# Performance work log

Hardware: AMD Instinct MI355X
Metric: run time of the kernel (lower is better)

## Reference

```python
import jax, jax.numpy as jnp
import numpy as np

EPS = 1e-12  # matches torch F.normalize eps

def _l2norm(x):
    n = jnp.linalg.norm(x, axis=-1, keepdims=True)
    return x / jnp.maximum(n, EPS)

def setup_inputs() -> dict:
    key = jax.random.key(0)
    k1, k2, k3, k4, k5 = jax.random.split(key, 5)
    B, S, D, V, N = 8, 512, 128, 100000, 2048
    query_embeddings = jax.random.normal(k1, (B, S, D), dtype=jnp.float32)
    key_embeddings = jax.random.normal(k2, (V, D), dtype=jnp.float32)
    batch_idx = jax.random.randint(k3, (N, 1), 0, B)
    seq_idx = jax.random.randint(k4, (N, 1), 0, S)
    label_locations = jnp.concatenate([batch_idx, seq_idx], axis=1).astype(jnp.int64)
    labels = jax.random.randint(k5, (N,), 0, V).astype(jnp.int64)
    return {"query_embeddings": query_embeddings, "key_embeddings": key_embeddings,
            "label_locations": label_locations, "labels": labels}

def reference(query_embeddings, key_embeddings, label_locations, labels):
    # gather supervised positions: [N, D]
    q = query_embeddings[label_locations[:, 0], label_locations[:, 1]]
    q = _l2norm(q)
    k = _l2norm(key_embeddings)
    logits = jnp.einsum('nd,vd->nv', q, k)  # [N, V]
    # mean-reduced softmax cross entropy
    logz = jax.nn.logsumexp(logits, axis=-1)  # [N]
    tgt = jnp.take_along_axis(logits, labels[:, None], axis=-1)[:, 0]
    return jnp.mean(logz - tgt)
```

## Files before the change

kernel.cpp:

```cpp
#include <hip/hip_runtime.h>
#include <hip/hip_bf16.h>

typedef __attribute__((ext_vector_type(8))) short short8;
typedef __attribute__((ext_vector_type(4))) short short4v;
typedef __attribute__((ext_vector_type(4))) float f32x4;

namespace {
constexpr int D    = 128;
constexpr int SEQ  = 512;
constexpr int NV   = 100000;
constexpr int NN   = 2048;
constexpr int KC   = 64;
constexpr int CHUNK_B = KC * D * 2;
constexpr int NCHUNK  = (NV + KC - 1) / KC;
constexpr int CPS     = 17;
constexpr int NSLICE  = (NCHUNK + CPS - 1) / CPS;
constexpr int MBLKS   = 8;
constexpr float LOG2E = 1.4426950408889634f;
constexpr float EPSN  = 1e-12f;
}

__global__ __launch_bounds__(256)
void prep_kernel(const float* __restrict__ qemb,
                 const float* __restrict__ kemb,
                 const int*   __restrict__ loc,
                 __hip_bfloat16* __restrict__ Kn,
                 __hip_bfloat16* __restrict__ Qn)
{
    const int gw   = (blockIdx.x * blockDim.x + threadIdx.x) >> 6;
    const int lane = threadIdx.x & 63;
    const int half = lane >> 5;
    const int l32  = lane & 31;
    const int row  = gw * 2 + half;
    if (row >= NV + NN) return;

    const float* src;
    __hip_bfloat16* dst;
    float extra;
    if (row < NV) {
        src = kemb + (size_t)row * D;
        dst = Kn + (size_t)row * D;
        extra = 1.0f;
    } else {
        int n = row - NV;
        int b = loc[2 * n], s = loc[2 * n + 1];
        src = qemb + ((size_t)b * SEQ + s) * D;
        dst = Qn + (size_t)n * D;
        extra = LOG2E;
    }
    float4 v = *(const float4*)(src + l32 * 4);
    float ss = v.x * v.x + v.y * v.y + v.z * v.z + v.w * v.w;
    #pragma unroll
    for (int m = 1; m < 32; m <<= 1) ss += __shfl_xor(ss, m);
    float inv = extra / fmaxf(sqrtf(ss), EPSN);

    union { __hip_bfloat162 h2[2]; short4v s4; } u;
    u.h2[0].x = __float2bfloat16(v.x * inv);
    u.h2[0].y = __float2bfloat16(v.y * inv);
    u.h2[1].x = __float2bfloat16(v.z * inv);
    u.h2[1].y = __float2bfloat16(v.w * inv);
    *(short4v*)((char*)dst + l32 * 8) = u.s4;
}

__global__ __launch_bounds__(512, 4)
void lse_main(const __hip_bfloat16* __restrict__ Kn,
              const __hip_bfloat16* __restrict__ Qn,
              float* __restrict__ sums)
{
    __shared__ char lds[3 * CHUNK_B];
    const int tid  = threadIdx.x;
    const int lane = tid & 63;
    const int lr   = lane & 15;
    const int lh   = lane >> 4;
    const int w    = tid >> 6;

    const int bid = blockIdx.x;
    const int lin = (bid & 7) * NSLICE + (bid >> 3);
    const int slice = lin >> 3;
    const int mblk  = lin & 7;

    const int chunk0 = slice * CPS;
    const int nch = min(CPS, NCHUNK - chunk0);
    const int m0 = mblk * 256 + w * 32;
    const char* kbase = (const char*)Kn;

    auto stage = [&](int c, int bi) {
        const int keybase = (chunk0 + c) * KC;
        #pragma unroll
        for (int r = 0; r < 2; ++r) {
            const int i   = w * 2 + r;
            const int kic = i * 4 + lh;
            const int key = min(keybase + kic, NV - 1);
            const int sb  = (lr ^ (kic & 7)) << 4;
            const char* g = kbase + (size_t)key * 256 + sb;
            const char* l = lds + bi * CHUNK_B + i * 1024;
            __builtin_amdgcn_global_load_lds(
                (const __attribute__((address_space(1))) void*)g,
                (__attribute__((address_space(3))) void*)l, 16, 0, 0);
        }
    };

    stage(0, 0);
    if (nch > 1) stage(1, 1);

    short8 qf[2][4];
    #pragma unroll
    for (int rg = 0; rg < 2; ++rg)
        #pragma unroll
        for (int ds = 0; ds < 4; ++ds)
            qf[rg][ds] = *(const short8*)((const short*)Qn +
                          (size_t)(m0 + rg * 16 + lr) * D + ds * 32 + lh * 8);

    float rowsum[2][4] = {};
    __syncthreads();

    for (int c = 0; c < nch; ++c) {
        if (c + 2 < nch) stage(c + 2, (c + 2) % 3);

        const char* buf = lds + (c % 3) * CHUNK_B;
        const int vbase = (chunk0 + c) * KC;
        const bool full = (vbase + KC <= NV);
        #pragma unroll
        for (int kg = 0; kg < 4; ++kg) {
            const int kic = kg * 16 + lr;
            const int rx  = (kic & 7) << 4;
            f32x4 acc[2] = {{0,0,0,0},{0,0,0,0}};
            #pragma unroll
            for (int ds2 = 0; ds2 < 4; ++ds2) {
                short8 bf = *(const short8*)(buf +
                              ((kic * 256 + ds2 * 64 + lh * 16) ^ rx));
                #pragma unroll
                for (int rg = 0; rg < 2; ++rg)
                    acc[rg] = __builtin_amdgcn_mfma_f32_16x16x32_bf16(
                                  qf[rg][ds2], bf, acc[rg], 0, 0, 0);
            }
            if (full) {
                #pragma unroll
                for (int rg = 0; rg < 2; ++rg)
                    #pragma unroll
                    for (int j = 0; j < 4; ++j)
                        rowsum[rg][j] += __builtin_amdgcn_exp2f(acc[rg][j]);
            } else {
                const bool ok = (vbase + kic) < NV;
                #pragma unroll
                for (int rg = 0; rg < 2; ++rg)
                    #pragma unroll
                    for (int j = 0; j < 4; ++j)
                        rowsum[rg][j] += ok ? __builtin_amdgcn_exp2f(acc[rg][j]) : 0.f;
            }
        }
        asm volatile("s_waitcnt vmcnt(2)" ::: "memory");
        __builtin_amdgcn_s_barrier();
        asm volatile("" ::: "memory");
    }

    #pragma unroll
    for (int rg = 0; rg < 2; ++rg)
        #pragma unroll
        for (int j = 0; j < 4; ++j) {
            float v = rowsum[rg][j];
            v += __shfl_xor(v, 1);
            v += __shfl_xor(v, 2);
            v += __shfl_xor(v, 4);
            v += __shfl_xor(v, 8);
            if (lr == 0)
                atomicAdd(&sums[m0 + rg * 16 + lh * 4 + j], v);
        }
}

__global__ void tgt_kernel(const float* __restrict__ qemb,
                           const float* __restrict__ kemb,
                           const int*   __restrict__ loc,
                           const int*   __restrict__ labels,
                           float* __restrict__ tgt)
{
    int n = (blockIdx.x * blockDim.x + threadIdx.x) >> 6;
    int lane = threadIdx.x & 63;
    if (n >= NN) return;
    int b = loc[2 * n], s = loc[2 * n + 1];
    const float* q = qemb + ((size_t)b * SEQ + s) * D;
    const float* k = kemb + (size_t)labels[n] * D;
    float2 qv = *(const float2*)(q + lane * 2);
    float2 kv = *(const float2*)(k + lane * 2);
    float qq = qv.x * qv.x + qv.y * qv.y;
    float kk = kv.x * kv.x + kv.y * kv.y;
    float qk = qv.x * kv.x + qv.y * kv.y;
    #pragma unroll
    for (int m = 1; m < 64; m <<= 1) {
        qq += __shfl_xor(qq, m);
        kk += __shfl_xor(kk, m);
        qk += __shfl_xor(qk, m);
    }
    if (lane == 0)
        tgt[n] = qk / (fmaxf(sqrtf(qq), EPSN) * fmaxf(sqrtf(kk), EPSN));
}

__global__ void final_kernel(const float* __restrict__ sums,
                             const float* __restrict__ tgt,
                             float* __restrict__ out)
{
    __shared__ float wsum[4];
    int t = threadIdx.x;
    float acc = 0.f;
    for (int n = t; n < NN; n += 256)
        acc += logf(sums[n]) - tgt[n];
    #pragma unroll
    for (int m = 1; m < 64; m <<= 1) acc += __shfl_xor(acc, m);
    if ((t & 63) == 0) wsum[t >> 6] = acc;
    __syncthreads();
    if (t == 0) out[0] = (wsum[0] + wsum[1] + wsum[2] + wsum[3]) / (float)NN;
}

extern "C" void kernel_launch(void* const* d_in, const int* in_sizes, int n_in,
                              void* d_out, int out_size, void* d_ws, size_t ws_size,
                              hipStream_t stream)
{
    const float* qemb   = (const float*)d_in[0];
    const float* kemb   = (const float*)d_in[1];
    const int*   loc    = (const int*)d_in[2];
    const int*   labels = (const int*)d_in[3];
    float* out = (float*)d_out;

    char* ws = (char*)d_ws;
    __hip_bfloat16* Kn = (__hip_bfloat16*)ws;
    size_t off = (size_t)NV * D * 2;
    __hip_bfloat16* Qn = (__hip_bfloat16*)(ws + off);
    off += (size_t)NN * D * 2;
    float* sums = (float*)(ws + off); off += (size_t)NN * 4;
    float* tgt  = (float*)(ws + off); off += (size_t)NN * 4;

    hipMemsetAsync(sums, 0, NN * sizeof(float), stream);

    {
        int waves  = (NV + NN + 1) / 2;
        int blocks = (waves + 3) / 4;
        prep_kernel<<<blocks, 256, 0, stream>>>(qemb, kemb, loc, Kn, Qn);
    }
    lse_main<<<MBLKS * NSLICE, 512, 0, stream>>>(Kn, Qn, sums);
    tgt_kernel<<<(NN * 64 + 255) / 256, 256, 0, stream>>>(qemb, kemb, loc, labels, tgt);
    final_kernel<<<1, 256, 0, stream>>>(sums, tgt, out);
}
```

Baseline: 161.0 us.

## Fuse target/final kernels into prep and main, enlarge per-wave tile and pipeline depth

The memset, target-logit kernel and final reduction kernel are removed. Zeroing and target dot products move into the prep kernel, and the final mean is computed by the last block of the LSE kernel using an atomic ticket counter. The main kernel now uses 256 threads with each wave covering 64 query rows, which doubles reuse of each staged key fragment. It also uses a four-buffer LDS pipeline with three chunks in flight and fixed slices of 25 chunks. This cuts launch overhead and LDS reads per MFMA, at the cost of more registers, larger LDS per block and a grid-wide completion counter.

```diff
diff --git a/kernel.cpp b/kernel.cpp
--- a/kernel.cpp
+++ b/kernel.cpp
@@ -12,10 +12,10 @@
 constexpr int NN   = 2048;
 constexpr int KC   = 64;
 constexpr int CHUNK_B = KC * D * 2;
-constexpr int NCHUNK  = (NV + KC - 1) / KC;
-constexpr int CPS     = 17;
-constexpr int NSLICE  = (NCHUNK + CPS - 1) / CPS;
+constexpr int CPS     = 25;
+constexpr int NSLICE  = 63;
 constexpr int MBLKS   = 8;
+constexpr int GRID    = MBLKS * NSLICE;
 constexpr float LOG2E = 1.4426950408889634f;
 constexpr float EPSN  = 1e-12f;
 }
@@ -24,50 +24,75 @@
 void prep_kernel(const float* __restrict__ qemb,
                  const float* __restrict__ kemb,
                  const int*   __restrict__ loc,
+                 const int*   __restrict__ labels,
                  __hip_bfloat16* __restrict__ Kn,
-                 __hip_bfloat16* __restrict__ Qn)
+                 __hip_bfloat16* __restrict__ Qn,
+                 float* __restrict__ tgt,
+                 float* __restrict__ sums,
+                 unsigned int* __restrict__ counter)
 {
-    const int gw   = (blockIdx.x * blockDim.x + threadIdx.x) >> 6;
+    const int gid = blockIdx.x * blockDim.x + threadIdx.x;
+    if (gid < NN) sums[gid] = 0.f;
+    if (gid == NN) *counter = 0u;
+
+    const int gw   = gid >> 6;
     const int lane = threadIdx.x & 63;
     const int half = lane >> 5;
     const int l32  = lane & 31;
     const int row  = gw * 2 + half;
     if (row >= NV + NN) return;
 
-    const float* src;
-    __hip_bfloat16* dst;
-    float extra;
     if (row < NV) {
-        src = kemb + (size_t)row * D;
-        dst = Kn + (size_t)row * D;
-        extra = 1.0f;
+        const float* src = kemb + (size_t)row * D;
+        float4 v = *(const float4*)(src + l32 * 4);
+        float ss = v.x * v.x + v.y * v.y + v.z * v.z + v.w * v.w;
+        #pragma unroll
+        for (int m = 1; m < 32; m <<= 1) ss += __shfl_xor(ss, m);
+        float inv = 1.0f / fmaxf(sqrtf(ss), EPSN);
+        union { __hip_bfloat162 h2[2]; short4v s4; } u;
+        u.h2[0].x = __float2bfloat16(v.x * inv);
+        u.h2[0].y = __float2bfloat16(v.y * inv);
+        u.h2[1].x = __float2bfloat16(v.z * inv);
+        u.h2[1].y = __float2bfloat16(v.w * inv);
+        *(short4v*)((char*)(Kn + (size_t)row * D) + l32 * 8) = u.s4;
     } else {
-        int n = row - NV;
-        int b = loc[2 * n], s = loc[2 * n + 1];
-        src = qemb + ((size_t)b * SEQ + s) * D;
-        dst = Qn + (size_t)n * D;
-        extra = LOG2E;
-    }
-    float4 v = *(const float4*)(src + l32 * 4);
-    float ss = v.x * v.x + v.y * v.y + v.z * v.z + v.w * v.w;
-    #pragma unroll
-    for (int m = 1; m < 32; m <<= 1) ss += __shfl_xor(ss, m);
-    float inv = extra / fmaxf(sqrtf(ss), EPSN);
-
-    union { __hip_bfloat162 h2[2]; short4v s4; } u;
-    u.h2[0].x = __float2bfloat16(v.x * inv);
-    u.h2[0].y = __float2bfloat16(v.y * inv);
-    u.h2[1].x = __float2bfloat16(v.z * inv);
-    u.h2[1].y = __float2bfloat16(v.w * inv);
-    *(short4v*)((char*)dst + l32 * 8) = u.s4;
-}
-
-__global__ __launch_bounds__(512, 4)
+        const int n = row - NV;
+        const int b = loc[2 * n], s = loc[2 * n + 1];
+        const float* q = qemb + ((size_t)b * SEQ + s) * D;
+        const float* k = kemb + (size_t)labels[n] * D;
+        float4 qv = *(const float4*)(q + l32 * 4);
+        float4 kv = *(const float4*)(k + l32 * 4);
+        float qq = qv.x * qv.x + qv.y * qv.y + qv.z * qv.z + qv.w * qv.w;
+        float kk = kv.x * kv.x + kv.y * kv.y + kv.z * kv.z + kv.w * kv.w;
+        float qk = qv.x * kv.x + qv.y * kv.y + qv.z * kv.z + qv.w * kv.w;
+        #pragma unroll
+        for (int m = 1; m < 32; m <<= 1) {
+            qq += __shfl_xor(qq, m);
+            kk += __shfl_xor(kk, m);
+            qk += __shfl_xor(qk, m);
+        }
+        float invq = 1.0f / fmaxf(sqrtf(qq), EPSN);
+        float scl  = LOG2E * invq;
+        union { __hip_bfloat162 h2[2]; short4v s4; } u;
+        u.h2[0].x = __float2bfloat16(qv.x * scl);
+        u.h2[0].y = __float2bfloat16(qv.y * scl);
+        u.h2[1].x = __float2bfloat16(qv.z * scl);
+        u.h2[1].y = __float2bfloat16(qv.w * scl);
+        *(short4v*)((char*)(Qn + (size_t)n * D) + l32 * 8) = u.s4;
+        if (l32 == 0)
+            tgt[n] = qk * invq / fmaxf(sqrtf(kk), EPSN);
+    }
+}
+
+__global__ __launch_bounds__(256, 2)
 void lse_main(const __hip_bfloat16* __restrict__ Kn,
               const __hip_bfloat16* __restrict__ Qn,
-              float* __restrict__ sums)
+              const float* __restrict__ tgt,
+              float* __restrict__ sums,
+              unsigned int* __restrict__ counter,
+              float* __restrict__ out)
 {
-    __shared__ char lds[3 * CHUNK_B];
+    __shared__ char lds[4 * CHUNK_B];
     const int tid  = threadIdx.x;
     const int lane = tid & 63;
     const int lr   = lane & 15;
@@ -80,15 +105,14 @@
     const int mblk  = lin & 7;
 
     const int chunk0 = slice * CPS;
-    const int nch = min(CPS, NCHUNK - chunk0);
-    const int m0 = mblk * 256 + w * 32;
+    const int m0 = mblk * 256 + w * 64;
     const char* kbase = (const char*)Kn;
 
     auto stage = [&](int c, int bi) {
         const int keybase = (chunk0 + c) * KC;
         #pragma unroll
-        for (int r = 0; r < 2; ++r) {
-            const int i   = w * 2 + r;
+        for (int r = 0; r < 4; ++r) {
+            const int i   = w * 4 + r;
             const int kic = i * 4 + lh;
             const int key = min(keybase + kic, NV - 1);
             const int sb  = (lr ^ (kic & 7)) << 4;
@@ -100,62 +124,71 @@
         }
     };
 
-    stage(0, 0);
-    if (nch > 1) stage(1, 1);
-
-    short8 qf[2][4];
+    stage(0, 0); stage(1, 1); stage(2, 2);
+
+    short8 qf[4][4];
     #pragma unroll
-    for (int rg = 0; rg < 2; ++rg)
+    for (int rg = 0; rg < 4; ++rg)
         #pragma unroll
         for (int ds = 0; ds < 4; ++ds)
             qf[rg][ds] = *(const short8*)((const short*)Qn +
                           (size_t)(m0 + rg * 16 + lr) * D + ds * 32 + lh * 8);
 
-    float rowsum[2][4] = {};
+    float rowsum[4][4] = {};
     __syncthreads();
 
-    for (int c = 0; c < nch; ++c) {
-        if (c + 2 < nch) stage(c + 2, (c + 2) % 3);
-
-        const char* buf = lds + (c % 3) * CHUNK_B;
+    for (int c = 0; c < CPS; ++c) {
+        if (c + 3 < CPS) stage(c + 3, (c + 3) & 3);
+
+        const char* buf = lds + (c & 3) * CHUNK_B;
         const int vbase = (chunk0 + c) * KC;
         const bool full = (vbase + KC <= NV);
         #pragma unroll
         for (int kg = 0; kg < 4; ++kg) {
             const int kic = kg * 16 + lr;
             const int rx  = (kic & 7) << 4;
-            f32x4 acc[2] = {{0,0,0,0},{0,0,0,0}};
+            f32x4 acc[4] = {{0,0,0,0},{0,0,0,0},{0,0,0,0},{0,0,0,0}};
             #pragma unroll
             for (int ds2 = 0; ds2 < 4; ++ds2) {
                 short8 bf = *(const short8*)(buf +
                               ((kic * 256 + ds2 * 64 + lh * 16) ^ rx));
                 #pragma unroll
-                for (int rg = 0; rg < 2; ++rg)
+                for (int rg = 0; rg < 4; ++rg)
                     acc[rg] = __builtin_amdgcn_mfma_f32_16x16x32_bf16(
                                   qf[rg][ds2], bf, acc[rg], 0, 0, 0);
             }
             if (full) {
                 #pragma unroll
-                for (int rg = 0; rg < 2; ++rg)
+                for (int rg = 0; rg < 4; ++rg)
                     #pragma unroll
                     for (int j = 0; j < 4; ++j)
                         rowsum[rg][j] += __builtin_amdgcn_exp2f(acc[rg][j]);
             } else {
                 const bool ok = (vbase + kic) < NV;
                 #pragma unroll
-                for (int rg = 0; rg < 2; ++rg)
+                for (int rg = 0; rg < 4; ++rg)
                     #pragma unroll
                     for (int j = 0; j < 4; ++j)
                         rowsum[rg][j] += ok ? __builtin_amdgcn_exp2f(acc[rg][j]) : 0.f;
             }
         }
-        asm volatile("s_waitcnt vmcnt(2)" ::: "memory");
-        __builtin_amdgcn_s_barrier();
-        asm volatile("" ::: "memory");
+        if (c < CPS - 3) {
+            asm volatile("s_waitcnt vmcnt(8)" ::: "memory");
+            __builtin_amdgcn_s_barrier();
+            asm volatile("" ::: "memory");
+        } else if (c == CPS - 3) {
+            asm volatile("s_waitcnt vmcnt(4)" ::: "memory");
+            __builtin_amdgcn_s_barrier();
+            asm volatile("" ::: "memory");
+        } else if (c == CPS - 2) {
+            asm volatile("s_waitcnt vmcnt(0)" ::: "memory");
+            __builtin_amdgcn_s_barrier();
+            asm volatile("" ::: "memory");
+        }
     }
 
     #pragma unroll
-    for (int rg = 0; rg < 2; ++rg)
+    for (int rg = 0; rg < 4; ++rg)
         #pragma unroll
         for (int j = 0; j < 4; ++j) {
             float v = rowsum[rg][j];
@@ -166,49 +199,28 @@
             if (lr == 0)
                 atomicAdd(&sums[m0 + rg * 16 + lh * 4 + j], v);
         }
-}
-
-__global__ void tgt_kernel(const float* __restrict__ qemb,
-                           const float* __restrict__ kemb,
-                           const int*   __restrict__ loc,
-                           const int*   __restrict__ labels,
-                           float* __restrict__ tgt)
-{
-    int n = (blockIdx.x * blockDim.x + threadIdx.x) >> 6;
-    int lane = threadIdx.x & 63;
-    if (n >= NN) return;
-    int b = loc[2 * n], s = loc[2 * n + 1];
-    const float* q = qemb + ((size_t)b * SEQ + s) * D;
-    const float* k = kemb + (size_t)labels[n] * D;
-    float2 qv = *(const float2*)(q + lane * 2);
-    float2 kv = *(const float2*)(k + lane * 2);
-    float qq = qv.x * qv.x + qv.y * qv.y;
-    float kk = kv.x * kv.x + kv.y * kv.y;
-    float qk = qv.x * kv.x + qv.y * kv.y;
-    #pragma unroll
-    for (int m = 1; m < 64; m <<= 1) {
-        qq += __shfl_xor(qq, m);
-        kk += __shfl_xor(kk, m);
-        qk += __shfl_xor(qk, m);
-    }
-    if (lane == 0)
-        tgt[n] = qk / (fmaxf(sqrtf(qq), EPSN) * fmaxf(sqrtf(kk), EPSN));
-}
-
-__global__ void final_kernel(const float* __restrict__ sums,
-                             const float* __restrict__ tgt,
-                             float* __restrict__ out)
-{
-    __shared__ float wsum[4];
-    int t = threadIdx.x;
-    float acc = 0.f;
-    for (int n = t; n < NN; n += 256)
-        acc += logf(sums[n]) - tgt[n];
-    #pragma unroll
-    for (int m = 1; m < 64; m <<= 1) acc += __shfl_xor(acc, m);
-    if ((t & 63) == 0) wsum[t >> 6] = acc;
+
+    __threadfence();
     __syncthreads();
-    if (t == 0) out[0] = (wsum[0] + wsum[1] + wsum[2] + wsum[3]) / (float)NN;
+    __shared__ int ticket_s;
+    if (tid == 0) ticket_s = (int)atomicAdd(counter, 1u);
+    __syncthreads();
+    if (ticket_s == GRID - 1) {
+        __threadfence();
+        __shared__ float wsum[4];
+        float acc = 0.f;
+        for (int n = tid; n < NN; n += 256) {
+            float sv = __hip_atomic_load(&sums[n], __ATOMIC_RELAXED,
+                                         __HIP_MEMORY_SCOPE_AGENT);
+            acc += logf(sv) - tgt[n];
+        }
+        #pragma unroll
+        for (int m = 1; m < 64; m <<= 1) acc += __shfl_xor(acc, m);
+        if ((tid & 63) == 0) wsum[tid >> 6] = acc;
+        __syncthreads();
+        if (tid == 0)
+            out[0] = (wsum[0] + wsum[1] + wsum[2] + wsum[3]) / (float)NN;
+    }
 }
 
 extern "C" void kernel_launch(void* const* d_in, const int* in_sizes, int n_in,
@@ -228,15 +240,13 @@
     off += (size_t)NN * D * 2;
     float* sums = (float*)(ws + off); off += (size_t)NN * 4;
     float* tgt  = (float*)(ws + off); off += (size_t)NN * 4;
-
-    hipMemsetAsync(sums, 0, NN * sizeof(float), stream);
+    unsigned int* counter = (unsigned int*)(ws + off);
 
     {
         int waves  = (NV + NN + 1) / 2;
         int blocks = (waves + 3) / 4;
-        prep_kernel<<<blocks, 256, 0, stream>>>(qemb, kemb, loc, Kn, Qn);
-    }
-    lse_main<<<MBLKS * NSLICE, 512, 0, stream>>>(Kn, Qn, sums);
-    tgt_kernel<<<(NN * 64 + 255) / 256, 256, 0, stream>>>(qemb, kemb, loc, labels, tgt);
-    final_kernel<<<1, 256, 0, stream>>>(sums, tgt, out);
-}
+        prep_kernel<<<blocks, 256, 0, stream>>>(qemb, kemb, loc, labels,
+                                                Kn, Qn, tgt, sums, counter);
+    }
+    lse_main<<<GRID, 256, 0, stream>>>(Kn, Qn, tgt, sums, counter, out);
+}
```

Result: slower. 186.1 us (+15.5%).
